# Kernel tuning notes

Hardware: AMD Instinct MI355X
Metric: run time of the kernel (lower is better)

## Reference

```python
import jax, jax.numpy as jnp
import numpy as np

GRID_SHAPE = (32, 32)
TEMPERATURE = 1.0


def setup_inputs() -> dict:
    key = jax.random.key(0)
    k1, k2 = jax.random.split(key)
    x = jax.random.normal(k1, (16384, 1024), dtype=jnp.float32)
    som_weights = jax.random.normal(k2, (*GRID_SHAPE, 1024), dtype=jnp.float32) * 0.05
    return {"x": x, "som_weights": som_weights}


def reference(x, som_weights):
    # x: [B, D]; som_weights: [G1, G2, D]
    B, D = x.shape
    g1, g2 = GRID_SHAPE
    w_flat = som_weights.reshape(g1 * g2, D)  # [N, D]
    x_sq = jnp.sum(x * x, axis=-1, keepdims=True)          # [B, 1]
    w_sq = jnp.sum(w_flat * w_flat, axis=-1)[None, :]       # [1, N]
    d2 = x_sq - 2.0 * (x @ w_flat.T) + w_sq                 # [B, N]
    logits = (-d2 / TEMPERATURE).reshape(B, g1, g2)         # [B, G1, G2]
    # per-dimension softmax along each spatial axis, combined multiplicatively
    s1 = jax.nn.softmax(logits, axis=1)
    s2 = jax.nn.softmax(logits, axis=2)
    combined = s1 * s2
    combined = combined / (jnp.sum(combined, axis=(1, 2), keepdims=True) + 1e-8)
    # soft reconstruction: weighted sum over grid of codebook vectors
    recon = jnp.einsum('bn,nd->bd', combined.reshape(B, g1 * g2), w_flat)
    return recon
```

## Files before the change

### kernel.cpp

```cpp
#include <hip/hip_runtime.h>

static constexpr int BATCH = 16384;
static constexpr int DIM   = 1024;
static constexpr int NN    = 1024;

typedef _Float16 half8  __attribute__((ext_vector_type(8)));
typedef _Float16 half4v __attribute__((ext_vector_type(4)));
typedef float    f32x4  __attribute__((ext_vector_type(4)));

static constexpr float L2E = 1.44269504088896340736f;

__global__ __launch_bounds__(256) void prep_kernel(const float* __restrict__ W,
                                                   _Float16* __restrict__ P1,
                                                   _Float16* __restrict__ P2,
                                                   float* __restrict__ wsq) {
    const int t = threadIdx.x;
    const int l = t & 63;
    const int v = t >> 6;
    const int f = blockIdx.x * 4 + v;
    const int hi = f >> 5, lo = f & 31;
    {
        int n  = hi * 16 + (l & 15);
        int k0 = lo * 32 + (l >> 4) * 8;
        const float* src = W + (size_t)n * DIM + k0;
        f32x4 a = *(const f32x4*)src;
        f32x4 b = *(const f32x4*)(src + 4);
        half8 h;
#pragma unroll
        for (int q = 0; q < 4; ++q) { h[q] = (_Float16)a[q]; h[4 + q] = (_Float16)b[q]; }
        *(half8*)(P1 + ((size_t)f * 64 + l) * 8) = h;
    }
    {
        int d  = hi * 16 + (l & 15);
        int n0 = lo * 32 + (l >> 4) * 8;
        half8 h;
#pragma unroll
        for (int j = 0; j < 8; ++j) h[j] = (_Float16)W[(size_t)(n0 + j) * DIM + d];
        *(half8*)(P2 + ((size_t)f * 64 + l) * 8) = h;
    }
    {
        const int row = blockIdx.x * 2 + (t >> 7);
        const int tt  = t & 127;
        const float* src = W + (size_t)row * DIM + tt * 8;
        f32x4 a = *(const f32x4*)src;
        f32x4 b = *(const f32x4*)(src + 4);
        float ss = a[0]*a[0] + a[1]*a[1] + a[2]*a[2] + a[3]*a[3]
                 + b[0]*b[0] + b[1]*b[1] + b[2]*b[2] + b[3]*b[3];
#pragma unroll
        for (int o = 32; o > 0; o >>= 1) ss += __shfl_xor(ss, o, 64);
        __shared__ float wred[4];
        if (l == 0) wred[v] = ss;
        __syncthreads();
        if (t == 0)   wsq[row] = L2E * (wred[0] + wred[1]);
        if (t == 128) wsq[row] = L2E * (wred[2] + wred[3]);
    }
}

__global__ __launch_bounds__(1024, 4) void fused_som_kernel(
    const float* __restrict__ X, const _Float16* __restrict__ P1,
    const _Float16* __restrict__ P2, const float* __restrict__ wsq,
    float* __restrict__ Out) {

    __shared__ __align__(16) _Float16 xs[2][64 * 64];
    __shared__ __align__(16) char     BIG[131072];
    __shared__ __align__(16) float    a1_lds[64 * 32];
    __shared__ __align__(16) float    rowred[16 * 64];
    __shared__ __align__(16) float    rowinv[64];

    const int t  = threadIdx.x;
    const int l  = t & 63;
    const int w  = t >> 6;
    const int r0 = blockIdx.x * 64;

    auto RIDX = [](int wv, int row, int g2) {
        return (wv * 64 + row) * 32 + (g2 ^ ((row & 4) << 2));
    };
    auto AIDX = [](int row, int g2) {
        return row * 32 + (g2 ^ ((row & 4) << 2));
    };

    const int srow = t >> 4;
    const int skq  = t & 15;

    auto xload = [&](int kt) -> f32x4 {
        return __builtin_nontemporal_load(
            (const f32x4*)(X + (size_t)(r0 + srow) * DIM + kt + skq * 4));
    };
    auto xwrite = [&](int buf, f32x4 v) {
        half4v h;
        h[0] = (_Float16)v[0]; h[1] = (_Float16)v[1];
        h[2] = (_Float16)v[2]; h[3] = (_Float16)v[3];
        int c = skq >> 1;
        *(half4v*)&xs[buf][srow * 64 + ((c ^ (srow & 7)) << 3) + ((skq & 1) << 2)] = h;
    };

    f32x4 acc[4][4] = {};
    {
        f32x4 xv = xload(0);
        xwrite(0, xv);
    }
    __syncthreads();

    for (int kt = 0; kt < DIM; kt += 64) {
        const int cur = (kt >> 6) & 1;
        const bool hasNext = (kt + 64 < DIM);
        f32x4 xv;
        if (hasNext) xv = xload(kt + 64);

        const int tk0 = kt >> 5;
        half8 bf0[4], bf1[4];
#pragma unroll
        for (int ni = 0; ni < 4; ++ni) {
            const size_t fb = (size_t)(w * 4 + ni) * 32;
            bf0[ni] = *(const half8*)(P1 + ((fb + tk0) * 64 + l) * 8);
            bf1[ni] = *(const half8*)(P1 + ((fb + tk0 + 1) * 64 + l) * 8);
        }
        half8 af[4];
#pragma unroll
        for (int mi = 0; mi < 4; ++mi) {
            const _Float16* pa = &xs[cur][((l & 15) + mi * 16) * 64];
            af[mi] = *(const half8*)(pa + (((l >> 4)) ^ (l & 7)) * 8);
        }
        __builtin_amdgcn_s_setprio(1);
#pragma unroll
        for (int mi = 0; mi < 4; ++mi)
#pragma unroll
            for (int ni = 0; ni < 4; ++ni)
                acc[mi][ni] = __builtin_amdgcn_mfma_f32_16x16x32_f16(
                    af[mi], bf0[ni], acc[mi][ni], 0, 0, 0);
        __builtin_amdgcn_s_setprio(0);
#pragma unroll
        for (int mi = 0; mi < 4; ++mi) {
            const _Float16* pa = &xs[cur][((l & 15) + mi * 16) * 64];
            af[mi] = *(const half8*)(pa + ((4 + (l >> 4)) ^ (l & 7)) * 8);
        }
        __builtin_amdgcn_s_setprio(1);
#pragma unroll
        for (int mi = 0; mi < 4; ++mi)
#pragma unroll
            for (int ni = 0; ni < 4; ++ni)
                acc[mi][ni] = __builtin_amdgcn_mfma_f32_16x16x32_f16(
                    af[mi], bf1[ni], acc[mi][ni], 0, 0, 0);
        __builtin_amdgcn_s_setprio(0);
        __builtin_amdgcn_sched_barrier(0);
        if (hasNext) xwrite(cur ^ 1, xv);
        __syncthreads();
    }

    float wq[4];
#pragma unroll
    for (int ni = 0; ni < 4; ++ni) wq[ni] = wsq[w * 64 + ni * 16 + (l & 15)];
#pragma unroll
    for (int mi = 0; mi < 4; ++mi)
#pragma unroll
        for (int ni = 0; ni < 4; ++ni)
#pragma unroll
            for (int q = 0; q < 4; ++q)
                acc[mi][ni][q] = exp2f(fmaf(acc[mi][ni][q], 2.0f * L2E, -wq[ni]));

    f32x4 rS2[4][2];
#pragma unroll
    for (int mi = 0; mi < 4; ++mi)
#pragma unroll
        for (int p = 0; p < 2; ++p) {
#pragma unroll
            for (int q = 0; q < 4; ++q) {
                float s = acc[mi][2 * p][q] + acc[mi][2 * p + 1][q];
                s += __shfl_xor(s, 1, 64);
                s += __shfl_xor(s, 2, 64);
                s += __shfl_xor(s, 4, 64);
                s += __shfl_xor(s, 8, 64);
                rS2[mi][p][q] = __builtin_amdgcn_rcpf(s);
            }
        }

    float* red = (float*)BIG;
#pragma unroll
    for (int mi = 0; mi < 4; ++mi)
#pragma unroll
        for (int j = 0; j < 2; ++j)
#pragma unroll
            for (int q = 0; q < 4; ++q) {
                int row = mi * 16 + (l >> 4) * 4 + q;
                red[RIDX(w, row, j * 16 + (l & 15))] =
                    acc[mi][j][q] + acc[mi][2 + j][q];
            }
    __syncthreads();
#pragma unroll
    for (int i = 0; i < 2; ++i) {
        int pr = t + i * 1024;
        int row = pr >> 5, g2 = pr & 31;
        float s = 0.f;
#pragma unroll
        for (int wv = 0; wv < 16; ++wv) s += red[RIDX(wv, row, g2)];
        a1_lds[AIDX(row, g2)] = __builtin_amdgcn_rcpf(s);
    }
    __syncthreads();

    _Float16* cs = (_Float16*)BIG;
#pragma unroll
    for (int mi = 0; mi < 4; ++mi) {
        f32x4 rs = {0.f, 0.f, 0.f, 0.f};
#pragma unroll
        for (int j = 0; j < 2; ++j) {
            f32x4 a1v;
#pragma unroll
            for (int q = 0; q < 4; ++q) {
                int row = mi * 16 + (l >> 4) * 4 + q;
                a1v[q] = a1_lds[AIDX(row, j * 16 + (l & 15))];
            }
#pragma unroll
            for (int p = 0; p < 2; ++p) {
                int ni  = 2 * p + j;
                int col = w * 64 + ni * 16 + (l & 15);
                int chunk = col >> 3;
#pragma unroll
                for (int q = 0; q < 4; ++q) {
                    float e = acc[mi][ni][q];
                    float cu = ((e * e) * a1v[q]) * rS2[mi][p][q];
                    rs[q] += cu;
                    int row = mi * 16 + (l >> 4) * 4 + q;
                    cs[row * 1024 + ((chunk ^ (row & 7)) << 3) + (col & 7)] =
                        (_Float16)cu;
                }
            }
        }
#pragma unroll
        for (int q = 0; q < 4; ++q) {
            float sv = rs[q];
            sv += __shfl_xor(sv, 1, 64);
            sv += __shfl_xor(sv, 2, 64);
            sv += __shfl_xor(sv, 4, 64);
            sv += __shfl_xor(sv, 8, 64);
            if ((l & 15) == 0) rowred[w * 64 + mi * 16 + (l >> 4) * 4 + q] = sv;
        }
    }
    __syncthreads();

    if (t < 64) {
        float tot = 0.f;
#pragma unroll
        for (int wv = 0; wv < 16; ++wv) tot += rowred[wv * 64 + t];
        rowinv[t] = 1.f / (tot + 1e-8f);
    }

    f32x4 acc2[4][4] = {};
#pragma unroll 2
    for (int kt = 0; kt < NN; kt += 32) {
        const int tn = kt >> 5;
        half8 bf[4], af2[4];
#pragma unroll
        for (int ni = 0; ni < 4; ++ni)
            bf[ni] = *(const half8*)(P2 +
                (((size_t)(w * 4 + ni) * 32 + tn) * 64 + l) * 8);
#pragma unroll
        for (int mi = 0; mi < 4; ++mi) {
            int row = (l & 15) + mi * 16;
            int kc  = tn * 4 + (l >> 4);
            af2[mi] = *(const half8*)(cs + row * 1024 + ((kc ^ (row & 7)) << 3));
        }
        __builtin_amdgcn_s_setprio(1);
#pragma unroll
        for (int mi = 0; mi < 4; ++mi)
#pragma unroll
            for (int ni = 0; ni < 4; ++ni)
                acc2[mi][ni] = __builtin_amdgcn_mfma_f32_16x16x32_f16(
                    af2[mi], bf[ni], acc2[mi][ni], 0, 0, 0);
        __builtin_amdgcn_s_setprio(0);
    }

    __syncthreads();
    float* stg = (float*)BIG;
#pragma unroll
    for (int half = 0; half < 2; ++half) {
        if (half) __syncthreads();
#pragma unroll
        for (int mm = 0; mm < 2; ++mm) {
            const int mi = half * 2 + mm;
#pragma unroll
            for (int ni = 0; ni < 4; ++ni) {
                const int col = w * 64 + ni * 16 + (l & 15);
#pragma unroll
                for (int q = 0; q < 4; ++q) {
                    const int rr = (l >> 4) * 4 + q;
                    const float inv = rowinv[mi * 16 + rr];
                    stg[(mm * 16 + rr) * 1024 + (col ^ ((rr & 4) << 2))] =
                        acc2[mi][ni][q] * inv;
                }
            }
        }
        __syncthreads();
#pragma unroll
        for (int i = 0; i < 8; ++i) {
            const int c  = t + i * 1024;
            const int rr = c >> 8;
            const int c4 = c & 255;
            f32x4 v = *(const f32x4*)&stg[rr * 1024 + ((c4 * 4) ^ ((rr & 4) << 2))];
            *(f32x4*)(Out + (size_t)(r0 + half * 32 + rr) * DIM + c4 * 4) = v;
        }
    }
}

extern "C" void kernel_launch(void* const* d_in, const int* in_sizes, int n_in,
                              void* d_out, int out_size, void* d_ws, size_t ws_size,
                              hipStream_t stream) {
    const float* x = (const float*)d_in[0];
    const float* w = (const float*)d_in[1];
    float* out = (float*)d_out;

    char* ws = (char*)d_ws;
    size_t off = 0;
    _Float16* pack1 = (_Float16*)(ws + off); off += (size_t)NN * DIM * 2;
    _Float16* pack2 = (_Float16*)(ws + off); off += (size_t)DIM * NN * 2;
    float*    wsq   = (float*)   (ws + off); off += (size_t)NN * 4;

    prep_kernel<<<512, 256, 0, stream>>>(w, pack1, pack2, wsq);
    fused_som_kernel<<<BATCH / 64, 1024, 0, stream>>>(x, pack1, pack2, wsq, out);
}
```

Before: 203.6 us.

## Shrink fused SOM tile to 32 rows with 512 threads and wider per-wave N

Each block now processes 32 batch rows with 8 waves instead of 64 rows with 16 waves. Each wave covers 128 codebook columns with a 2x8 MFMA tile instead of 4x4, which halves LDS use and lets more blocks fit per CU and gives a 512-block grid. In exchange, every block rereads the full packed codebook for half as many rows, doubling the global/L2 traffic for P1 and P2 per output row. Output stores also become nontemporal.

```diff
diff --git a/kernel.cpp b/kernel.cpp
--- a/kernel.cpp
+++ b/kernel.cpp
@@ -56,24 +56,24 @@
     }
 }
 
-__global__ __launch_bounds__(1024, 4) void fused_som_kernel(
+__global__ __launch_bounds__(512, 4) void fused_som_kernel(
     const float* __restrict__ X, const _Float16* __restrict__ P1,
     const _Float16* __restrict__ P2, const float* __restrict__ wsq,
     float* __restrict__ Out) {
 
-    __shared__ __align__(16) _Float16 xs[2][64 * 64];
-    __shared__ __align__(16) char     BIG[131072];
-    __shared__ __align__(16) float    a1_lds[64 * 32];
-    __shared__ __align__(16) float    rowred[16 * 64];
-    __shared__ __align__(16) float    rowinv[64];
+    __shared__ __align__(16) _Float16 xs[2][32 * 64];
+    __shared__ __align__(16) char     BIG[65536];
+    __shared__ __align__(16) float    a1_lds[32 * 32];
+    __shared__ __align__(16) float    rowred[8 * 32];
+    __shared__ __align__(16) float    rowinv[32];
 
     const int t  = threadIdx.x;
     const int l  = t & 63;
     const int w  = t >> 6;
-    const int r0 = blockIdx.x * 64;
+    const int r0 = blockIdx.x * 32;
 
     auto RIDX = [](int wv, int row, int g2) {
-        return (wv * 64 + row) * 32 + (g2 ^ ((row & 4) << 2));
+        return (wv * 32 + row) * 32 + (g2 ^ ((row & 4) << 2));
     };
     auto AIDX = [](int row, int g2) {
         return row * 32 + (g2 ^ ((row & 4) << 2));
@@ -94,7 +94,7 @@
         *(half4v*)&xs[buf][srow * 64 + ((c ^ (srow & 7)) << 3) + ((skq & 1) << 2)] = h;
     };
 
-    f32x4 acc[4][4] = {};
+    f32x4 acc[2][8] = {};
     {
         f32x4 xv = xload(0);
         xwrite(0, xv);
@@ -108,61 +108,62 @@
         if (hasNext) xv = xload(kt + 64);
 
         const int tk0 = kt >> 5;
-        half8 bf0[4], bf1[4];
-#pragma unroll
-        for (int ni = 0; ni < 4; ++ni) {
-            const size_t fb = (size_t)(w * 4 + ni) * 32;
-            bf0[ni] = *(const half8*)(P1 + ((fb + tk0) * 64 + l) * 8);
-            bf1[ni] = *(const half8*)(P1 + ((fb + tk0 + 1) * 64 + l) * 8);
-        }
-        half8 af[4];
-#pragma unroll
-        for (int mi = 0; mi < 4; ++mi) {
+        half8 bf[8], af[2];
+#pragma unroll
+        for (int ni = 0; ni < 8; ++ni)
+            bf[ni] = *(const half8*)(P1 +
+                (((size_t)(w * 8 + ni) * 32 + tk0) * 64 + l) * 8);
+#pragma unroll
+        for (int mi = 0; mi < 2; ++mi) {
             const _Float16* pa = &xs[cur][((l & 15) + mi * 16) * 64];
             af[mi] = *(const half8*)(pa + (((l >> 4)) ^ (l & 7)) * 8);
         }
         __builtin_amdgcn_s_setprio(1);
 #pragma unroll
-        for (int mi = 0; mi < 4; ++mi)
-#pragma unroll
-            for (int ni = 0; ni < 4; ++ni)
+        for (int mi = 0; mi < 2; ++mi)
+#pragma unroll
+            for (int ni = 0; ni < 8; ++ni)
                 acc[mi][ni] = __builtin_amdgcn_mfma_f32_16x16x32_f16(
-                    af[mi], bf0[ni], acc[mi][ni], 0, 0, 0);
+                    af[mi], bf[ni], acc[mi][ni], 0, 0, 0);
         __builtin_amdgcn_s_setprio(0);
 #pragma unroll
-        for (int mi = 0; mi < 4; ++mi) {
+        for (int ni = 0; ni < 8; ++ni)
+            bf[ni] = *(const half8*)(P1 +
+                (((size_t)(w * 8 + ni) * 32 + tk0 + 1) * 64 + l) * 8);
+#pragma unroll
+        for (int mi = 0; mi < 2; ++mi) {
             const _Float16* pa = &xs[cur][((l & 15) + mi * 16) * 64];
             af[mi] = *(const half8*)(pa + ((4 + (l >> 4)) ^ (l & 7)) * 8);
         }
         __builtin_amdgcn_s_setprio(1);
 #pragma unroll
-        for (int mi = 0; mi < 4; ++mi)
-#pragma unroll
-            for (int ni = 0; ni < 4; ++ni)
+        for (int mi = 0; mi < 2; ++mi)
+#pragma unroll
+            for (int ni = 0; ni < 8; ++ni)
                 acc[mi][ni] = __builtin_amdgcn_mfma_f32_16x16x32_f16(
-                    af[mi], bf1[ni], acc[mi][ni], 0, 0, 0);
+                    af[mi], bf[ni], acc[mi][ni], 0, 0, 0);
         __builtin_amdgcn_s_setprio(0);
         __builtin_amdgcn_sched_barrier(0);
         if (hasNext) xwrite(cur ^ 1, xv);
         __syncthreads();
     }
 
-    float wq[4];
-#pragma unroll
-    for (int ni = 0; ni < 4; ++ni) wq[ni] = wsq[w * 64 + ni * 16 + (l & 15)];
-#pragma unroll
-    for (int mi = 0; mi < 4; ++mi)
-#pragma unroll
-        for (int ni = 0; ni < 4; ++ni)
+    float wq[8];
+#pragma unroll
+    for (int ni = 0; ni < 8; ++ni) wq[ni] = wsq[w * 128 + ni * 16 + (l & 15)];
+#pragma unroll
+    for (int mi = 0; mi < 2; ++mi)
+#pragma unroll
+        for (int ni = 0; ni < 8; ++ni)
 #pragma unroll
             for (int q = 0; q < 4; ++q)
                 acc[mi][ni][q] = exp2f(fmaf(acc[mi][ni][q], 2.0f * L2E, -wq[ni]));
 
-    f32x4 rS2[4][2];
-#pragma unroll
-    for (int mi = 0; mi < 4; ++mi)
-#pragma unroll
-        for (int p = 0; p < 2; ++p) {
+    f32x4 rS2[2][4];
+#pragma unroll
+    for (int mi = 0; mi < 2; ++mi)
+#pragma unroll
+        for (int p = 0; p < 4; ++p) {
 #pragma unroll
             for (int q = 0; q < 4; ++q) {
                 float s = acc[mi][2 * p][q] + acc[mi][2 * p + 1][q];
@@ -176,30 +177,31 @@
 
     float* red = (float*)BIG;
 #pragma unroll
-    for (int mi = 0; mi < 4; ++mi)
+    for (int mi = 0; mi < 2; ++mi)
 #pragma unroll
         for (int j = 0; j < 2; ++j)
 #pragma unroll
             for (int q = 0; q < 4; ++q) {
                 int row = mi * 16 + (l >> 4) * 4 + q;
                 red[RIDX(w, row, j * 16 + (l & 15))] =
-                    acc[mi][j][q] + acc[mi][2 + j][q];
+                    (acc[mi][j][q]     + acc[mi][2 + j][q]) +
+                    (acc[mi][4 + j][q] + acc[mi][6 + j][q]);
             }
     __syncthreads();
 #pragma unroll
     for (int i = 0; i < 2; ++i) {
-        int pr = t + i * 1024;
+        int pr = t + i * 512;
         int row = pr >> 5, g2 = pr & 31;
         float s = 0.f;
 #pragma unroll
-        for (int wv = 0; wv < 16; ++wv) s += red[RIDX(wv, row, g2)];
+        for (int wv = 0; wv < 8; ++wv) s += red[RIDX(wv, row, g2)];
         a1_lds[AIDX(row, g2)] = __builtin_amdgcn_rcpf(s);
     }
     __syncthreads();
 
     _Float16* cs = (_Float16*)BIG;
 #pragma unroll
-    for (int mi = 0; mi < 4; ++mi) {
+    for (int mi = 0; mi < 2; ++mi) {
         f32x4 rs = {0.f, 0.f, 0.f, 0.f};
 #pragma unroll
         for (int j = 0; j < 2; ++j) {
@@ -210,9 +212,9 @@
                 a1v[q] = a1_lds[AIDX(row, j * 16 + (l & 15))];
             }
 #pragma unroll
-            for (int p = 0; p < 2; ++p) {
+            for (int p = 0; p < 4; ++p) {
                 int ni  = 2 * p + j;
-                int col = w * 64 + ni * 16 + (l & 15);
+                int col = w * 128 + ni * 16 + (l & 15);
                 int chunk = col >> 3;
 #pragma unroll
                 for (int q = 0; q < 4; ++q) {
@@ -232,38 +234,36 @@
             sv += __shfl_xor(sv, 2, 64);
             sv += __shfl_xor(sv, 4, 64);
             sv += __shfl_xor(sv, 8, 64);
-            if ((l & 15) == 0) rowred[w * 64 + mi * 16 + (l >> 4) * 4 + q] = sv;
-        }
-    }
-    __syncthreads();
-
-    if (t < 64) {
+            if ((l & 15) == 0) rowred[w * 32 + mi * 16 + (l >> 4) * 4 + q] = sv;
+        }
+    }
+    __syncthreads();
+
+    if (t < 32) {
         float tot = 0.f;
 #pragma unroll
-        for (int wv = 0; wv < 16; ++wv) tot += rowred[wv * 64 + t];
+        for (int wv = 0; wv < 8; ++wv) tot += rowred[wv * 32 + t];
         rowinv[t] = 1.f / (tot + 1e-8f);
     }
 
-    f32x4 acc2[4][4] = {};
-#pragma unroll 2
-    for (int kt = 0; kt < NN; kt += 32) {
-        const int tn = kt >> 5;
-        half8 bf[4], af2[4];
-#pragma unroll
-        for (int ni = 0; ni < 4; ++ni)
+    f32x4 acc2[2][8] = {};
+    for (int tn = 0; tn < 32; ++tn) {
+        half8 bf[8], af2[2];
+#pragma unroll
+        for (int ni = 0; ni < 8; ++ni)
             bf[ni] = *(const half8*)(P2 +
-                (((size_t)(w * 4 + ni) * 32 + tn) * 64 + l) * 8);
-#pragma unroll
-        for (int mi = 0; mi < 4; ++mi) {
+                (((size_t)(w * 8 + ni) * 32 + tn) * 64 + l) * 8);
+#pragma unroll
+        for (int mi = 0; mi < 2; ++mi) {
             int row = (l & 15) + mi * 16;
             int kc  = tn * 4 + (l >> 4);
             af2[mi] = *(const half8*)(cs + row * 1024 + ((kc ^ (row & 7)) << 3));
         }
         __builtin_amdgcn_s_setprio(1);
 #pragma unroll
-        for (int mi = 0; mi < 4; ++mi)
-#pragma unroll
-            for (int ni = 0; ni < 4; ++ni)
+        for (int mi = 0; mi < 2; ++mi)
+#pragma unroll
+            for (int ni = 0; ni < 8; ++ni)
                 acc2[mi][ni] = __builtin_amdgcn_mfma_f32_16x16x32_f16(
                     af2[mi], bf[ni], acc2[mi][ni], 0, 0, 0);
         __builtin_amdgcn_s_setprio(0);
@@ -274,29 +274,27 @@
 #pragma unroll
     for (int half = 0; half < 2; ++half) {
         if (half) __syncthreads();
-#pragma unroll
-        for (int mm = 0; mm < 2; ++mm) {
-            const int mi = half * 2 + mm;
-#pragma unroll
-            for (int ni = 0; ni < 4; ++ni) {
-                const int col = w * 64 + ni * 16 + (l & 15);
-#pragma unroll
-                for (int q = 0; q < 4; ++q) {
-                    const int rr = (l >> 4) * 4 + q;
-                    const float inv = rowinv[mi * 16 + rr];
-                    stg[(mm * 16 + rr) * 1024 + (col ^ ((rr & 4) << 2))] =
-                        acc2[mi][ni][q] * inv;
-                }
+        const int mi = half;
+#pragma unroll
+        for (int ni = 0; ni < 8; ++ni) {
+            const int col = w * 128 + ni * 16 + (l & 15);
+#pragma unroll
+            for (int q = 0; q < 4; ++q) {
+                const int rr = (l >> 4) * 4 + q;
+                const float inv = rowinv[mi * 16 + rr];
+                stg[rr * 1024 + (col ^ ((rr & 4) << 2))] =
+                    acc2[mi][ni][q] * inv;
             }
         }
         __syncthreads();
 #pragma unroll
         for (int i = 0; i < 8; ++i) {
-            const int c  = t + i * 1024;
+            const int c  = t + i * 512;
             const int rr = c >> 8;
             const int c4 = c & 255;
             f32x4 v = *(const f32x4*)&stg[rr * 1024 + ((c4 * 4) ^ ((rr & 4) << 2))];
-            *(f32x4*)(Out + (size_t)(r0 + half * 32 + rr) * DIM + c4 * 4) = v;
+            __builtin_nontemporal_store(v,
+                (f32x4*)(Out + (size_t)(r0 + half * 16 + rr) * DIM + c4 * 4));
         }
     }
 }
@@ -315,5 +313,5 @@
     float*    wsq   = (float*)   (ws + off); off += (size_t)NN * 4;
 
     prep_kernel<<<512, 256, 0, stream>>>(w, pack1, pack2, wsq);
-    fused_som_kernel<<<BATCH / 64, 1024, 0, stream>>>(x, pack1, pack2, wsq, out);
+    fused_som_kernel<<<BATCH / 32, 512, 0, stream>>>(x, pack1, pack2, wsq, out);
 }
```

Result: slower. 276.2 us (+35.7%).
